# Performance work log

Hardware: AMD Instinct MI355X
Metric: run time of the kernel (lower is better)

Reference implementation:

```python
import jax, jax.numpy as jnp
import numpy as np

N = 25000        # nodes
E = 400000       # edges (before self-loops)
HEADS = 8
GROUPS = 8
F_IN = 256
HID = 64
N_CLASS = 32
N_LAYERS = 3


def grouped_linear(x, w, b):
    # x: [..., Cin], w: [G, Cin//G, Cout//G], b: [Cout]
    G = w.shape[0]
    xs = x.reshape(x.shape[:-1] + (G, -1))
    out = jnp.einsum('...gi,gio->...go', xs, w)
    return out.reshape(x.shape[:-1] + (-1,)) + b


def gcn_norm(edge_index, n):
    # PyG gcn_norm with add_self_loops=True, unit edge weights
    row = jnp.concatenate([edge_index[0], jnp.arange(n)])
    col = jnp.concatenate([edge_index[1], jnp.arange(n)])
    w = jnp.ones(row.shape[0], jnp.float32)
    deg = jax.ops.segment_sum(w, col, num_segments=n)
    dis = jnp.where(deg > 0, jax.lax.rsqrt(deg), 0.0)
    return row, col, dis[row] * w * dis[col]


def dna_conv(x_all, row, col, norm, wq, bq, wk, bk, wv, bv):
    # x_all: [N, L, H]; row/col/norm: [E'] (edges incl. self-loops)
    Ee = row.shape[0]
    L, H = x_all.shape[1], x_all.shape[2]
    dh = H // HEADS
    # query from target's latest state, key/value from full source history
    q = grouped_linear(x_all[col, -1:], wq, bq).reshape(Ee, 1, HEADS, dh).transpose(0, 2, 1, 3)
    k = grouped_linear(x_all[row], wk, bk).reshape(Ee, L, HEADS, dh).transpose(0, 2, 1, 3)
    v = grouped_linear(x_all[row], wv, bv).reshape(Ee, L, HEADS, dh).transpose(0, 2, 1, 3)
    attn = jax.nn.softmax(jnp.einsum('ehqd,ehld->ehql', q, k) / jnp.sqrt(jnp.float32(dh)), axis=-1)
    out = jnp.einsum('ehql,ehld->ehqd', attn, v)           # [E', HEADS, 1, dh]
    out = out.transpose(0, 2, 1, 3).reshape(Ee, H)          # [E', H]
    return jax.ops.segment_sum(norm[:, None] * out, col, num_segments=N)


def setup_inputs() -> dict:
    key = jax.random.key(0)
    ks = jax.random.split(key, 12)
    s = 0.2
    return {
        'x': jax.random.normal(ks[0], (N, F_IN), jnp.float32),
        'edge_index': jax.random.randint(ks[1], (2, E), 0, N),
        'lin1_w': jax.random.normal(ks[2], (F_IN, HID), jnp.float32) * 0.05,
        'lin1_b': jnp.zeros((HID,), jnp.float32),
        'wq': jax.random.normal(ks[3], (N_LAYERS, GROUPS, HID // GROUPS, HID // GROUPS), jnp.float32) * s,
        'bq': jnp.zeros((N_LAYERS, HID), jnp.float32),
        'wk': jax.random.normal(ks[4], (N_LAYERS, GROUPS, HID // GROUPS, HID // GROUPS), jnp.float32) * s,
        'bk': jnp.zeros((N_LAYERS, HID), jnp.float32),
        'wv': jax.random.normal(ks[5], (N_LAYERS, GROUPS, HID // GROUPS, HID // GROUPS), jnp.float32) * s,
        'bv': jnp.zeros((N_LAYERS, HID), jnp.float32),
        'lin2_w': jax.random.normal(ks[6], (HID, N_CLASS), jnp.float32) * 0.1,
        'lin2_b': jnp.zeros((N_CLASS,), jnp.float32),
    }


def reference(x, edge_index, lin1_w, lin1_b, wq, bq, wk, bk, wv, bv, lin2_w, lin2_b):
    row, col, norm = gcn_norm(edge_index, N)
    h = jax.nn.relu(x @ lin1_w + lin1_b)                    # [N, HID]; dropout = identity (eval)
    x_all = h[:, None, :]                                   # [N, 1, HID]
    for l in range(N_LAYERS):
        out = jax.nn.relu(dna_conv(x_all, row, col, norm,
                                   wq[l], bq[l], wk[l], bk[l], wv[l], bv[l]))
        x_all = jnp.concatenate([x_all, out[:, None, :]], axis=1)
    logits = x_all[:, -1] @ lin2_w + lin2_b                 # [N, N_CLASS]
    return jax.nn.log_softmax(logits, axis=1)
```

## Files before the change

kernel.cpp:

```cpp
#include <hip/hip_runtime.h>
#include <hip/hip_fp16.h>
#include <math.h>

#define NN 25000
#define NE 400000
#define HID 64
#define F_IN 256
#define N_CLASS 32
#define MAXL 4
#define KVS 3
#define WPAD 264
#define SCAN_NB 98

typedef _Float16 f16;
typedef _Float16 f16x2 __attribute__((ext_vector_type(2)));
typedef _Float16 f16x8 __attribute__((ext_vector_type(8)));
typedef float f32x4 __attribute__((ext_vector_type(4)));

union F16x8 {
    f16x8 v;
    f16x2 h[4];
    __half2 hh[4];
};

__device__ __forceinline__ float dot2(f16x2 a, f16x2 b, float c) {
#if __has_builtin(__builtin_amdgcn_fdot2)
    return __builtin_amdgcn_fdot2(a, b, c, false);
#else
    return c + (float)a[0] * (float)b[0] + (float)a[1] * (float)b[1];
#endif
}

__global__ void wprep_kernel(const float* __restrict__ w, f16* __restrict__ wt) {
    int e = blockIdx.x * blockDim.x + threadIdx.x;
    int k = e >> 6, nn = e & 63;
    wt[nn * F_IN + k] = (f16)w[e];
}

__global__ void __launch_bounds__(256) deg_lin1_kernel(
        const int* __restrict__ col, int* __restrict__ deg, int E, int degBlocks,
        const float* __restrict__ x, const f16x8* __restrict__ wt,
        const float* __restrict__ b, float* __restrict__ x_all, int n) {
    __shared__ f16 wlds[64 * WPAD];
    if (blockIdx.x < degBlocks) {
        int e = blockIdx.x * 256 + threadIdx.x;
        if (e < E) atomicAdd(&deg[col[e]], 1);
        return;
    }
    int bid = blockIdx.x - degBlocks;
    int t = threadIdx.x;
    #pragma unroll
    for (int j = 0; j < 8; ++j) {
        int idx = t + j * 256;
        int e = idx * 8;
        int nr = e >> 8, k0 = e & 255;
        *(f16x8*)&wlds[nr * WPAD + k0] = wt[idx];
    }
    __syncthreads();
    int wave = t >> 6, lane = t & 63;
    int m = lane & 15, quad = lane >> 4;
    int rowA = bid * 64 + wave * 16 + m;
    int rA = min(rowA, n - 1);
    const float* xp = x + (size_t)rA * F_IN + quad * 8;
    f32x4 acc[4] = {};
    for (int kk = 0; kk < F_IN; kk += 32) {
        float4 x0 = *(const float4*)(xp + kk);
        float4 x1 = *(const float4*)(xp + kk + 4);
        f16x8 a;
        a[0] = (f16)x0.x; a[1] = (f16)x0.y; a[2] = (f16)x0.z; a[3] = (f16)x0.w;
        a[4] = (f16)x1.x; a[5] = (f16)x1.y; a[6] = (f16)x1.z; a[7] = (f16)x1.w;
        #pragma unroll
        for (int nt = 0; nt < 4; ++nt) {
            f16x8 bf = *(const f16x8*)&wlds[(nt * 16 + m) * WPAD + kk + quad * 8];
            acc[nt] = __builtin_amdgcn_mfma_f32_16x16x32_f16(a, bf, acc[nt], 0, 0, 0);
        }
    }
    int rowC = bid * 64 + wave * 16 + quad * 4;
    #pragma unroll
    for (int nt = 0; nt < 4; ++nt) {
        int c2 = nt * 16 + m;
        float bias = b[c2];
        #pragma unroll
        for (int r = 0; r < 4; ++r) {
            int row = rowC + r;
            if (row < n)
                x_all[(size_t)row * (MAXL * HID) + c2] = fmaxf(acc[nt][r] + bias, 0.f);
        }
    }
}

__global__ void scanA_kernel(const int* __restrict__ deg, int* __restrict__ bsum, int n) {
    int t = threadIdx.x;
    int i = blockIdx.x * 256 + t;
    int v = (i < n) ? deg[i] : 0;
    #pragma unroll
    for (int off = 1; off < 64; off <<= 1) v += __shfl_xor(v, off);
    __shared__ int wsum[4];
    if ((t & 63) == 0) wsum[t >> 6] = v;
    __syncthreads();
    if (t == 0) bsum[blockIdx.x] = wsum[0] + wsum[1] + wsum[2] + wsum[3];
}

__global__ void scanC_kernel(const int* __restrict__ deg, const int* __restrict__ bsum,
                             int* __restrict__ rowptr, int* __restrict__ cursor,
                             float* __restrict__ dis, int n) {
    __shared__ int s[128];
    int t = threadIdx.x;
    {
        int v = (t < SCAN_NB) ? bsum[t] : 0;
        s[t] = v;
        __syncthreads();
        for (int off = 1; off < 128; off <<= 1) {
            int u = (t >= off) ? s[t - off] : 0;
            __syncthreads();
            s[t] += u;
            __syncthreads();
        }
    }
    int base = (blockIdx.x > 0) ? s[blockIdx.x - 1] : 0;
    __syncthreads();

    int i = blockIdx.x * 256 + t;
    int lane = t & 63, w = t >> 6;
    int v = (i < n) ? deg[i] : 0;
    int x = v;
    #pragma unroll
    for (int off = 1; off < 64; off <<= 1) {
        int u = __shfl_up(x, off);
        if (lane >= off) x += u;
    }
    __shared__ int wsum[4];
    if (lane == 63) wsum[w] = x;
    __syncthreads();
    for (int ww = 0; ww < w; ++ww) base += wsum[ww];
    if (i < n) {
        int excl = base + x - v;
        rowptr[i] = excl;
        cursor[i] = excl;
        dis[i] = rsqrtf((float)(v + 1));
    }
}

__global__ void scatter_t1_kernel(const int* __restrict__ row, const int* __restrict__ col,
                                  int* __restrict__ cursor, int* __restrict__ csr_src,
                                  int E, int scatBlocks,
                                  const float* __restrict__ x_all,
                                  const float* __restrict__ wv, const float* __restrict__ bv,
                                  const float* __restrict__ dis,
                                  f16x2* __restrict__ KV, int n) {
    if (blockIdx.x < scatBlocks) {
        int e = blockIdx.x * 256 + threadIdx.x;
        if (e >= E) return;
        int c = col[e];
        int p = atomicAdd(&cursor[c], 1);
        csr_src[p] = row[e];
        return;
    }
    int t = (blockIdx.x - scatBlocks) * 256 + threadIdx.x;
    int node = t >> 5, u = t & 31;
    if (node >= n) return;
    int g = u >> 2;
    int o0 = (u & 3) * 2;
    const float4* xg4 = (const float4*)(x_all + (size_t)node * (MAXL * HID) + g * 8);
    float4 xa = xg4[0], xb = xg4[1];
    float xv[8] = {xa.x, xa.y, xa.z, xa.w, xb.x, xb.y, xb.z, xb.w};
    float d = dis[node];
    const float* wgv = wv + g * 64;
    float v0 = bv[g * 8 + o0], v1 = bv[g * 8 + o0 + 1];
    #pragma unroll
    for (int i = 0; i < 8; ++i) {
        v0 = fmaf(xv[i], wgv[i * 8 + o0], v0);
        v1 = fmaf(xv[i], wgv[i * 8 + o0 + 1], v1);
    }
    f16x2 vh; vh[0] = (f16)(v0 * d); vh[1] = (f16)(v1 * d);
    KV[((size_t)node * KVS * 2 + 1) * 32 + u] = vh;
}

__global__ void gather1_kernel(const int* __restrict__ rowptr, const int* __restrict__ deg,
                               const int* __restrict__ csr_src, const float* __restrict__ dis,
                               const f16x8* __restrict__ KV8, float* __restrict__ x_all, int n) {
    int wave = (int)((blockIdx.x * (size_t)blockDim.x + threadIdx.x) >> 6);
    int lane = threadIdx.x & 63;
    if (wave >= n) return;
    int c = wave;
    int u = lane & 7;
    int slot = lane >> 3;
    float nc = dis[c];
    int beg = rowptr[c];
    int dc = deg[c] + 1;
    float acc[8];
    #pragma unroll
    for (int i = 0; i < 8; ++i) acc[i] = 0.f;

    for (int j = 0; j < dc; j += 32) {
        int jj0 = j + slot, jj1 = jj0 + 8, jj2 = jj0 + 16, jj3 = jj0 + 24;
        bool va0 = jj0 < dc, va1 = jj1 < dc, va2 = jj2 < dc, va3 = jj3 < dc;
        int r0 = c, r1 = c, r2 = c, r3 = c;
        if (va0 && jj0 > 0) r0 = csr_src[beg + jj0 - 1];
        if (va1)            r1 = csr_src[beg + jj1 - 1];
        if (va2)            r2 = csr_src[beg + jj2 - 1];
        if (va3)            r3 = csr_src[beg + jj3 - 1];
        F16x8 v0, v1, v2, v3;
        v0.v = KV8[(size_t)r0 * (KVS * 2 * 8) + 8 + u];
        v1.v = KV8[(size_t)r1 * (KVS * 2 * 8) + 8 + u];
        v2.v = KV8[(size_t)r2 * (KVS * 2 * 8) + 8 + u];
        v3.v = KV8[(size_t)r3 * (KVS * 2 * 8) + 8 + u];
        __half2 p0 = __float2half2_rn(va0 ? 1.f : 0.f);
        __half2 p1 = __float2half2_rn(va1 ? 1.f : 0.f);
        __half2 p2 = __float2half2_rn(va2 ? 1.f : 0.f);
        __half2 p3 = __float2half2_rn(va3 ? 1.f : 0.f);
        __half2 ha[4];
        #pragma unroll
        for (int i2 = 0; i2 < 4; ++i2) {
            ha[i2] = __hmul2(p0, v0.hh[i2]);
            ha[i2] = __hfma2(p1, v1.hh[i2], ha[i2]);
            ha[i2] = __hfma2(p2, v2.hh[i2], ha[i2]);
            ha[i2] = __hfma2(p3, v3.hh[i2], ha[i2]);
        }
        #pragma unroll
        for (int i2 = 0; i2 < 4; ++i2) {
            float2 f = __half22float2(ha[i2]);
            acc[i2 * 2]     += f.x;
            acc[i2 * 2 + 1] += f.y;
        }
    }
    #pragma unroll
    for (int off = 8; off < 64; off <<= 1) {
        #pragma unroll
        for (int i = 0; i < 8; ++i) acc[i] += __shfl_xor(acc[i], off);
    }
    if (slot == 0) {
        float4* dst = (float4*)(x_all + ((size_t)c * MAXL + 1) * HID + u * 8);
        dst[0] = make_float4(fmaxf(acc[0] * nc, 0.f), fmaxf(acc[1] * nc, 0.f),
                             fmaxf(acc[2] * nc, 0.f), fmaxf(acc[3] * nc, 0.f));
        dst[1] = make_float4(fmaxf(acc[4] * nc, 0.f), fmaxf(acc[5] * nc, 0.f),
                             fmaxf(acc[6] * nc, 0.f), fmaxf(acc[7] * nc, 0.f));
    }
}

__global__ void transform_kernel(const float* __restrict__ x_all,
                                 const float* __restrict__ wq, const float* __restrict__ bq,
                                 const float* __restrict__ wk, const float* __restrict__ bk,
                                 const float* __restrict__ wv, const float* __restrict__ bv,
                                 const float* __restrict__ dis,
                                 f16x2* __restrict__ Q2, f16x2* __restrict__ KV,
                                 int n, int L) {
    int t = blockIdx.x * blockDim.x + threadIdx.x;
    int node = t >> 5, u = t & 31;
    if (node >= n) return;
    int g = u >> 2;
    int o0 = (u & 3) * 2;
    const float* xrow = x_all + (size_t)node * (MAXL * HID);
    float d = dis[node];

    {
        const float4* xg4 = (const float4*)(xrow + (L - 1) * HID + g * 8);
        float4 xa = xg4[0], xb = xg4[1];
        float xv[8] = {xa.x, xa.y, xa.z, xa.w, xb.x, xb.y, xb.z, xb.w};
        const float* wg = wq + g * 64;
        float a0 = bq[g * 8 + o0], a1 = bq[g * 8 + o0 + 1];
        #pragma unroll
        for (int i = 0; i < 8; ++i) {
            a0 = fmaf(xv[i], wg[i * 8 + o0], a0);
            a1 = fmaf(xv[i], wg[i * 8 + o0 + 1], a1);
        }
        f16x2 q; q[0] = (f16)a0; q[1] = (f16)a1;
        Q2[(size_t)node * 32 + u] = q;
    }
    for (int ll = 0; ll < L; ++ll) {
        const float4* xg4 = (const float4*)(xrow + ll * HID + g * 8);
        float4 xa = xg4[0], xb = xg4[1];
        float xv[8] = {xa.x, xa.y, xa.z, xa.w, xb.x, xb.y, xb.z, xb.w};
        const float* wgk = wk + g * 64;
        const float* wgv = wv + g * 64;
        float k0 = bk[g * 8 + o0], k1 = bk[g * 8 + o0 + 1];
        float v0 = bv[g * 8 + o0], v1 = bv[g * 8 + o0 + 1];
        #pragma unroll
        for (int i = 0; i < 8; ++i) {
            k0 = fmaf(xv[i], wgk[i * 8 + o0], k0);
            k1 = fmaf(xv[i], wgk[i * 8 + o0 + 1], k1);
            v0 = fmaf(xv[i], wgv[i * 8 + o0], v0);
            v1 = fmaf(xv[i], wgv[i * 8 + o0 + 1], v1);
        }
        f16x2 kh; kh[0] = (f16)k0; kh[1] = (f16)k1;
        f16x2 vh; vh[0] = (f16)(v0 * d); vh[1] = (f16)(v1 * d);
        size_t base = ((size_t)node * KVS + ll) * 2;
        KV[(base + 0) * 32 + u] = kh;
        KV[(base + 1) * 32 + u] = vh;
    }
}

template <int L, bool FINAL>
__global__ void gather_kernel(const int* __restrict__ rowptr, const int* __restrict__ deg,
                              const int* __restrict__ csr_src, const float* __restrict__ dis,
                              const f16x8* __restrict__ Q8, const f16x8* __restrict__ KV8,
                              float* __restrict__ x_all,
                              const float* __restrict__ w2, const float* __restrict__ b2,
                              float* __restrict__ out, int n) {
    int wave = (int)((blockIdx.x * (size_t)blockDim.x + threadIdx.x) >> 6);
    int lane = threadIdx.x & 63;
    if (wave >= n) return;
    int c = wave;
    int u = lane & 7;
    int slot = lane >> 3;
    F16x8 q; q.v = Q8[(size_t)c * 8 + u];
    float nc = dis[c];
    int beg = rowptr[c];
    int dc = deg[c] + 1;
    float acc[8];
    #pragma unroll
    for (int i = 0; i < 8; ++i) acc[i] = 0.f;

    for (int j = 0; j < dc; j += 32) {
        int jj0 = j + slot;
        int jj1 = jj0 + 8;
        int jj2 = jj0 + 16;
        int jj3 = jj0 + 24;
        bool va0 = jj0 < dc, va1 = jj1 < dc, va2 = jj2 < dc, va3 = jj3 < dc;
        int r0 = c, r1 = c, r2 = c, r3 = c;
        if (va0 && jj0 > 0) r0 = csr_src[beg + jj0 - 1];
        if (va1)            r1 = csr_src[beg + jj1 - 1];
        if (va2)            r2 = csr_src[beg + jj2 - 1];
        if (va3)            r3 = csr_src[beg + jj3 - 1];

        size_t rb0 = (size_t)r0 * (KVS * 2 * 8);
        size_t rb1 = (size_t)r1 * (KVS * 2 * 8);
        size_t rb2 = (size_t)r2 * (KVS * 2 * 8);
        size_t rb3 = (size_t)r3 * (KVS * 2 * 8);
        F16x8 kk0[L], vv0[L], kk1[L], vv1[L], kk2[L], vv2[L], kk3[L], vv3[L];
        #pragma unroll
        for (int ll = 0; ll < L; ++ll) {
            kk0[ll].v = KV8[rb0 + ll * 16 + u];
            vv0[ll].v = KV8[rb0 + ll * 16 + 8 + u];
            kk1[ll].v = KV8[rb1 + ll * 16 + u];
            vv1[ll].v = KV8[rb1 + ll * 16 + 8 + u];
            kk2[ll].v = KV8[rb2 + ll * 16 + u];
            vv2[ll].v = KV8[rb2 + ll * 16 + 8 + u];
            kk3[ll].v = KV8[rb3 + ll * 16 + u];
            vv3[ll].v = KV8[rb3 + ll * 16 + 8 + u];
        }

        {
            float s0[L], s1[L];
            #pragma unroll
            for (int ll = 0; ll < L; ++ll) {
                float p0 = 0.f, p1 = 0.f;
                #pragma unroll
                for (int i2 = 0; i2 < 4; ++i2) {
                    p0 = dot2(q.h[i2], kk0[ll].h[i2], p0);
                    p1 = dot2(q.h[i2], kk1[ll].h[i2], p1);
                }
                s0[ll] = p0 * 0.35355339059327373f;
                s1[ll] = p1 * 0.35355339059327373f;
            }
            float m0 = s0[0], m1 = s1[0];
            #pragma unroll
            for (int ll = 1; ll < L; ++ll) { m0 = fmaxf(m0, s0[ll]); m1 = fmaxf(m1, s1[ll]); }
            float sum0 = 0.f, sum1 = 0.f;
            #pragma unroll
            for (int ll = 0; ll < L; ++ll) {
                s0[ll] = __expf(s0[ll] - m0); sum0 += s0[ll];
                s1[ll] = __expf(s1[ll] - m1); sum1 += s1[ll];
            }
            float inv0 = va0 ? 1.f / sum0 : 0.f;
            float inv1 = va1 ? 1.f / sum1 : 0.f;
            __half2 ha[4];
            #pragma unroll
            for (int i2 = 0; i2 < 4; ++i2) ha[i2] = __float2half2_rn(0.f);
            #pragma unroll
            for (int ll = 0; ll < L; ++ll) {
                __half2 p0 = __float2half2_rn(s0[ll] * inv0);
                __half2 p1 = __float2half2_rn(s1[ll] * inv1);
                #pragma unroll
                for (int i2 = 0; i2 < 4; ++i2) {
                    ha[i2] = __hfma2(p0, vv0[ll].hh[i2], ha[i2]);
                    ha[i2] = __hfma2(p1, vv1[ll].hh[i2], ha[i2]);
                }
            }
            #pragma unroll
            for (int i2 = 0; i2 < 4; ++i2) {
                float2 f = __half22float2(ha[i2]);
                acc[i2 * 2]     += f.x;
                acc[i2 * 2 + 1] += f.y;
            }
        }
        {
            float s0[L], s1[L];
            #pragma unroll
            for (int ll = 0; ll < L; ++ll) {
                float p0 = 0.f, p1 = 0.f;
                #pragma unroll
                for (int i2 = 0; i2 < 4; ++i2) {
                    p0 = dot2(q.h[i2], kk2[ll].h[i2], p0);
                    p1 = dot2(q.h[i2], kk3[ll].h[i2], p1);
                }
                s0[ll] = p0 * 0.35355339059327373f;
                s1[ll] = p1 * 0.35355339059327373f;
            }
            float m0 = s0[0], m1 = s1[0];
            #pragma unroll
            for (int ll = 1; ll < L; ++ll) { m0 = fmaxf(m0, s0[ll]); m1 = fmaxf(m1, s1[ll]); }
            float sum0 = 0.f, sum1 = 0.f;
            #pragma unroll
            for (int ll = 0; ll < L; ++ll) {
                s0[ll] = __expf(s0[ll] - m0); sum0 += s0[ll];
                s1[ll] = __expf(s1[ll] - m1); sum1 += s1[ll];
            }
            float inv0 = va2 ? 1.f / sum0 : 0.f;
            float inv1 = va3 ? 1.f / sum1 : 0.f;
            __half2 ha[4];
            #pragma unroll
            for (int i2 = 0; i2 < 4; ++i2) ha[i2] = __float2half2_rn(0.f);
            #pragma unroll
            for (int ll = 0; ll < L; ++ll) {
                __half2 p0 = __float2half2_rn(s0[ll] * inv0);
                __half2 p1 = __float2half2_rn(s1[ll] * inv1);
                #pragma unroll
                for (int i2 = 0; i2 < 4; ++i2) {
                    ha[i2] = __hfma2(p0, vv2[ll].hh[i2], ha[i2]);
                    ha[i2] = __hfma2(p1, vv3[ll].hh[i2], ha[i2]);
                }
            }
            #pragma unroll
            for (int i2 = 0; i2 < 4; ++i2) {
                float2 f = __half22float2(ha[i2]);
                acc[i2 * 2]     += f.x;
                acc[i2 * 2 + 1] += f.y;
            }
        }
    }
    #pragma unroll
    for (int off = 8; off < 64; off <<= 1) {
        #pragma unroll
        for (int i = 0; i < 8; ++i) acc[i] += __shfl_xor(acc[i], off);
    }

    if constexpr (!FINAL) {
        if (slot == 0) {
            float4* dst = (float4*)(x_all + ((size_t)c * MAXL + L) * HID + u * 8);
            dst[0] = make_float4(fmaxf(acc[0] * nc, 0.f), fmaxf(acc[1] * nc, 0.f),
                                 fmaxf(acc[2] * nc, 0.f), fmaxf(acc[3] * nc, 0.f));
            dst[1] = make_float4(fmaxf(acc[4] * nc, 0.f), fmaxf(acc[5] * nc, 0.f),
                                 fmaxf(acc[6] * nc, 0.f), fmaxf(acc[7] * nc, 0.f));
        }
    } else {
        float xn[8];
        #pragma unroll
        for (int i = 0; i < 8; ++i) xn[i] = fmaxf(acc[i] * nc, 0.f);
        float pl[4] = {0.f, 0.f, 0.f, 0.f};
        const float* w2p = w2 + (u * 8) * N_CLASS + slot * 4;
        #pragma unroll
        for (int i = 0; i < 8; ++i) {
            float4 wv4 = *(const float4*)(w2p + i * N_CLASS);
            pl[0] = fmaf(xn[i], wv4.x, pl[0]);
            pl[1] = fmaf(xn[i], wv4.y, pl[1]);
            pl[2] = fmaf(xn[i], wv4.z, pl[2]);
            pl[3] = fmaf(xn[i], wv4.w, pl[3]);
        }
        #pragma unroll
        for (int off = 1; off < 8; off <<= 1) {
            #pragma unroll
            for (int cc = 0; cc < 4; ++cc) pl[cc] += __shfl_xor(pl[cc], off);
        }
        float4 bb = *(const float4*)(b2 + slot * 4);
        pl[0] += bb.x; pl[1] += bb.y; pl[2] += bb.z; pl[3] += bb.w;
        float lm = fmaxf(fmaxf(pl[0], pl[1]), fmaxf(pl[2], pl[3]));
        #pragma unroll
        for (int off = 8; off < 64; off <<= 1) lm = fmaxf(lm, __shfl_xor(lm, off));
        float se = __expf(pl[0] - lm) + __expf(pl[1] - lm)
                 + __expf(pl[2] - lm) + __expf(pl[3] - lm);
        #pragma unroll
        for (int off = 8; off < 64; off <<= 1) se += __shfl_xor(se, off);
        float ls = logf(se);
        if (u == 0) {
            float4 o4 = make_float4(pl[0] - lm - ls, pl[1] - lm - ls,
                                    pl[2] - lm - ls, pl[3] - lm - ls);
            *(float4*)(out + (size_t)c * N_CLASS + slot * 4) = o4;
        }
    }
}

extern "C" void kernel_launch(void* const* d_in, const int* in_sizes, int n_in,
                              void* d_out, int out_size, void* d_ws, size_t ws_size,
                              hipStream_t stream) {
    const float* x      = (const float*)d_in[0];
    const int*   eidx   = (const int*)d_in[1];
    const float* lin1_w = (const float*)d_in[2];
    const float* lin1_b = (const float*)d_in[3];
    const float* wq     = (const float*)d_in[4];
    const float* bq     = (const float*)d_in[5];
    const float* wk     = (const float*)d_in[6];
    const float* bk     = (const float*)d_in[7];
    const float* wv     = (const float*)d_in[8];
    const float* bv     = (const float*)d_in[9];
    const float* lin2_w = (const float*)d_in[10];
    const float* lin2_b = (const float*)d_in[11];
    float* out = (float*)d_out;

    const int n  = NN;
    const int E  = NE;
    const int* row = eidx;
    const int* col = eidx + E;

    char* ws = (char*)d_ws;
    float*  x_all  = (float*)ws;   ws += (size_t)NN * MAXL * HID * 4;
    f16x2*  Q2     = (f16x2*)ws;   ws += (size_t)NN * 32 * 4;
    f16x2*  KV     = (f16x2*)ws;   ws += (size_t)NN * KVS * 2 * 32 * 4;
    float*  dis    = (float*)ws;   ws += (size_t)NN * 4;
    int*    deg    = (int*)ws;     ws += (size_t)NN * 4;
    int*    rowptr = (int*)ws;     ws += (size_t)NN * 4;
    int*    cursor = (int*)ws;     ws += (size_t)NN * 4;
    int*    csr    = (int*)ws;     ws += (size_t)NE * 4;
    f16*    wt16   = (f16*)ws;     ws += (size_t)HID * F_IN * 2;
    int*    bsum   = (int*)ws;     ws += 128 * 4;

    const int degBlocks  = (E + 255) / 256;
    const int lin1Blocks = (n + 63) / 64;
    const int t1Blocks   = (n * 32 + 255) / 256;
    const int blocks     = (n + 3) / 4;

    hipMemsetAsync(deg, 0, (size_t)NN * 4, stream);
    wprep_kernel<<<(HID * F_IN + 255) / 256, 256, 0, stream>>>(lin1_w, wt16);

    deg_lin1_kernel<<<degBlocks + lin1Blocks, 256, 0, stream>>>(
        col, deg, E, degBlocks, x, (const f16x8*)wt16, lin1_b, x_all, n);

    scanA_kernel<<<SCAN_NB, 256, 0, stream>>>(deg, bsum, n);
    scanC_kernel<<<SCAN_NB, 256, 0, stream>>>(deg, bsum, rowptr, cursor, dis, n);

    scatter_t1_kernel<<<degBlocks + t1Blocks, 256, 0, stream>>>(
        row, col, cursor, csr, E, degBlocks, x_all, wv, bv, dis, KV, n);

    gather1_kernel<<<blocks, 256, 0, stream>>>(rowptr, deg, csr, dis,
                                               (const f16x8*)KV, x_all, n);

    transform_kernel<<<t1Blocks, 256, 0, stream>>>(
        x_all, wq + 512, bq + 64, wk + 512, bk + 64, wv + 512, bv + 64,
        dis, Q2, KV, n, 2);
    gather_kernel<2, false><<<blocks, 256, 0, stream>>>(
        rowptr, deg, csr, dis, (const f16x8*)Q2, (const f16x8*)KV,
        x_all, lin2_w, lin2_b, out, n);

    transform_kernel<<<t1Blocks, 256, 0, stream>>>(
        x_all, wq + 1024, bq + 128, wk + 1024, bk + 128, wv + 1024, bv + 128,
        dis, Q2, KV, n, 3);
    gather_kernel<3, true><<<blocks, 256, 0, stream>>>(
        rowptr, deg, csr, dis, (const f16x8*)Q2, (const f16x8*)KV,
        x_all, lin2_w, lin2_b, out, n);
}
```

Baseline: 272.8 us.

## Schedule gather waves by descending node degree via bucketed permutation

Builds a degree histogram and bucket scan, then has scatter_t1 emit a permutation of nodes sorted by descending in-degree. The three gather kernels process nodes in that order so long-degree nodes start first and load balance across waves improves. The memset is also folded into a combined prep kernel. This adds a small kernel launch and an extra indirection, and the output and x_all writes become scattered rather than sequential.

```diff
diff --git a/kernel.cpp b/kernel.cpp
--- a/kernel.cpp
+++ b/kernel.cpp
@@ -31,10 +31,19 @@
 #endif
 }
 
-__global__ void wprep_kernel(const float* __restrict__ w, f16* __restrict__ wt) {
-    int e = blockIdx.x * blockDim.x + threadIdx.x;
-    int k = e >> 6, nn = e & 63;
-    wt[nn * F_IN + k] = (f16)w[e];
+__global__ void prep_kernel(const float* __restrict__ w, f16* __restrict__ wt,
+                            int* __restrict__ deg, int* __restrict__ dhist, int n) {
+    int b = blockIdx.x, t = threadIdx.x;
+    if (b < 64) {
+        int e = b * 256 + t;
+        int k = e >> 6, nn = e & 63;
+        wt[nn * F_IN + k] = (f16)w[e];
+    } else if (b < 64 + SCAN_NB) {
+        int i = (b - 64) * 256 + t;
+        if (i < n) deg[i] = 0;
+    } else {
+        dhist[t] = 0;
+    }
 }
 
 __global__ void __launch_bounds__(256) deg_lin1_kernel(
@@ -89,16 +98,37 @@
     }
 }
 
-__global__ void scanA_kernel(const int* __restrict__ deg, int* __restrict__ bsum, int n) {
+__global__ void scanA_kernel(const int* __restrict__ deg, int* __restrict__ bsum,
+                             int* __restrict__ dhist, int n) {
+    __shared__ int lh[256];
     int t = threadIdx.x;
+    lh[t] = 0;
+    __syncthreads();
     int i = blockIdx.x * 256 + t;
     int v = (i < n) ? deg[i] : 0;
+    if (i < n) atomicAdd(&lh[255 - min(v, 255)], 1);
     #pragma unroll
     for (int off = 1; off < 64; off <<= 1) v += __shfl_xor(v, off);
     __shared__ int wsum[4];
     if ((t & 63) == 0) wsum[t >> 6] = v;
     __syncthreads();
     if (t == 0) bsum[blockIdx.x] = wsum[0] + wsum[1] + wsum[2] + wsum[3];
+    if (lh[t]) atomicAdd(&dhist[t], lh[t]);
+}
+
+__global__ void bucketScan_kernel(const int* __restrict__ dhist, int* __restrict__ bcur) {
+    __shared__ int s[256];
+    int t = threadIdx.x;
+    int v = dhist[t];
+    s[t] = v;
+    __syncthreads();
+    for (int off = 1; off < 256; off <<= 1) {
+        int u = (t >= off) ? s[t - off] : 0;
+        __syncthreads();
+        s[t] += u;
+        __syncthreads();
+    }
+    bcur[t] = s[t] - v;
 }
 
 __global__ void scanC_kernel(const int* __restrict__ deg, const int* __restrict__ bsum,
@@ -147,7 +177,9 @@
                                   const float* __restrict__ x_all,
                                   const float* __restrict__ wv, const float* __restrict__ bv,
                                   const float* __restrict__ dis,
-                                  f16x2* __restrict__ KV, int n) {
+                                  f16x2* __restrict__ KV,
+                                  const int* __restrict__ deg, int* __restrict__ bcur,
+                                  int* __restrict__ perm, int n) {
     if (blockIdx.x < scatBlocks) {
         int e = blockIdx.x * 256 + threadIdx.x;
         if (e >= E) return;
@@ -159,6 +191,11 @@
     int t = (blockIdx.x - scatBlocks) * 256 + threadIdx.x;
     int node = t >> 5, u = t & 31;
     if (node >= n) return;
+    if (u == 0) {
+        int bb = 255 - min(deg[node], 255);
+        int p = atomicAdd(&bcur[bb], 1);
+        perm[p] = node;
+    }
     int g = u >> 2;
     int o0 = (u & 3) * 2;
     const float4* xg4 = (const float4*)(x_all + (size_t)node * (MAXL * HID) + g * 8);
@@ -176,13 +213,14 @@
     KV[((size_t)node * KVS * 2 + 1) * 32 + u] = vh;
 }
 
-__global__ void gather1_kernel(const int* __restrict__ rowptr, const int* __restrict__ deg,
+__global__ void gather1_kernel(const int* __restrict__ perm,
+                               const int* __restrict__ rowptr, const int* __restrict__ deg,
                                const int* __restrict__ csr_src, const float* __restrict__ dis,
                                const f16x8* __restrict__ KV8, float* __restrict__ x_all, int n) {
     int wave = (int)((blockIdx.x * (size_t)blockDim.x + threadIdx.x) >> 6);
     int lane = threadIdx.x & 63;
     if (wave >= n) return;
-    int c = wave;
+    int c = perm[wave];
     int u = lane & 7;
     int slot = lane >> 3;
     float nc = dis[c];
@@ -291,7 +329,8 @@
 }
 
 template <int L, bool FINAL>
-__global__ void gather_kernel(const int* __restrict__ rowptr, const int* __restrict__ deg,
+__global__ void gather_kernel(const int* __restrict__ perm,
+                              const int* __restrict__ rowptr, const int* __restrict__ deg,
                               const int* __restrict__ csr_src, const float* __restrict__ dis,
                               const f16x8* __restrict__ Q8, const f16x8* __restrict__ KV8,
                               float* __restrict__ x_all,
@@ -300,7 +339,7 @@
     int wave = (int)((blockIdx.x * (size_t)blockDim.x + threadIdx.x) >> 6);
     int lane = threadIdx.x & 63;
     if (wave >= n) return;
-    int c = wave;
+    int c = perm[wave];
     int u = lane & 7;
     int slot = lane >> 3;
     F16x8 q; q.v = Q8[(size_t)c * 8 + u];
@@ -513,38 +552,42 @@
     int*    csr    = (int*)ws;     ws += (size_t)NE * 4;
     f16*    wt16   = (f16*)ws;     ws += (size_t)HID * F_IN * 2;
     int*    bsum   = (int*)ws;     ws += 128 * 4;
+    int*    dhist  = (int*)ws;     ws += 256 * 4;
+    int*    bcur   = (int*)ws;     ws += 256 * 4;
+    int*    perm   = (int*)ws;     ws += (size_t)NN * 4;
 
     const int degBlocks  = (E + 255) / 256;
     const int lin1Blocks = (n + 63) / 64;
     const int t1Blocks   = (n * 32 + 255) / 256;
     const int blocks     = (n + 3) / 4;
 
-    hipMemsetAsync(deg, 0, (size_t)NN * 4, stream);
-    wprep_kernel<<<(HID * F_IN + 255) / 256, 256, 0, stream>>>(lin1_w, wt16);
+    prep_kernel<<<64 + SCAN_NB + 1, 256, 0, stream>>>(lin1_w, wt16, deg, dhist, n);
 
     deg_lin1_kernel<<<degBlocks + lin1Blocks, 256, 0, stream>>>(
         col, deg, E, degBlocks, x, (const f16x8*)wt16, lin1_b, x_all, n);
 
-    scanA_kernel<<<SCAN_NB, 256, 0, stream>>>(deg, bsum, n);
+    scanA_kernel<<<SCAN_NB, 256, 0, stream>>>(deg, bsum, dhist, n);
+    bucketScan_kernel<<<1, 256, 0, stream>>>(dhist, bcur);
     scanC_kernel<<<SCAN_NB, 256, 0, stream>>>(deg, bsum, rowptr, cursor, dis, n);
 
     scatter_t1_kernel<<<degBlocks + t1Blocks, 256, 0, stream>>>(
-        row, col, cursor, csr, E, degBlocks, x_all, wv, bv, dis, KV, n);
-
-    gather1_kernel<<<blocks, 256, 0, stream>>>(rowptr, deg, csr, dis,
+        row, col, cursor, csr, E, degBlocks, x_all, wv, bv, dis, KV,
+        deg, bcur, perm, n);
+
+    gather1_kernel<<<blocks, 256, 0, stream>>>(perm, rowptr, deg, csr, dis,
                                                (const f16x8*)KV, x_all, n);
 
     transform_kernel<<<t1Blocks, 256, 0, stream>>>(
         x_all, wq + 512, bq + 64, wk + 512, bk + 64, wv + 512, bv + 64,
         dis, Q2, KV, n, 2);
     gather_kernel<2, false><<<blocks, 256, 0, stream>>>(
-        rowptr, deg, csr, dis, (const f16x8*)Q2, (const f16x8*)KV,
+        perm, rowptr, deg, csr, dis, (const f16x8*)Q2, (const f16x8*)KV,
         x_all, lin2_w, lin2_b, out, n);
 
     transform_kernel<<<t1Blocks, 256, 0, stream>>>(
         x_all, wq + 1024, bq + 128, wk + 1024, bk + 128, wv + 1024, bv + 128,
         dis, Q2, KV, n, 3);
     gather_kernel<3, true><<<blocks, 256, 0, stream>>>(
-        rowptr, deg, csr, dis, (const f16x8*)Q2, (const f16x8*)KV,
+        perm, rowptr, deg, csr, dis, (const f16x8*)Q2, (const f16x8*)KV,
         x_all, lin2_w, lin2_b, out, n);
 }
```

Measured after the change: 387.1 us. 41.9% more time.
